# Optimization experiments

Measured on AMD Instinct MI355X. Metric: run time of the kernel, lower is better.

Reference implementation:

```python
import jax, jax.numpy as jnp
import numpy as np
import math

B, L, D, H, DK, DFF = 4, 1024, 1024, 16, 64, 4096
NUM_BUCKETS, MAX_DIST = 32, 128


def _relative_position_bucket(rel):
    # bidirectional T5 bucketing; rel = memory_pos - context_pos
    nb = NUM_BUCKETS // 2
    n = -rel
    ret = (n < 0).astype(jnp.int32) * nb
    n = jnp.abs(n)
    max_exact = nb // 2
    is_small = n < max_exact
    val_if_large = max_exact + (
        jnp.log(jnp.maximum(n, 1).astype(jnp.float32) / max_exact)
        / math.log(MAX_DIST / max_exact)
        * (nb - max_exact)
    ).astype(jnp.int32)
    val_if_large = jnp.minimum(val_if_large, nb - 1)
    return ret + jnp.where(is_small, n.astype(jnp.int32), val_if_large)


def t5_layernorm(x, w, eps):
    # no mean subtraction, no bias (T5 style)
    var = jnp.mean(jnp.square(x.astype(jnp.float32)), axis=-1, keepdims=True)
    return w * (x / jnp.sqrt(var + eps))


def setup_inputs() -> dict:
    key = jax.random.key(0)
    ks = jax.random.split(key, 12)
    inp = {
        "src": jax.random.normal(ks[0], (B, L, D), dtype=jnp.float32),
        "enc_position": jnp.broadcast_to(jnp.arange(L, dtype=jnp.int32), (B, L)),
        "ln1_w": jnp.ones((D,), jnp.float32),
        "wq": jax.random.normal(ks[1], (H * DK, D), jnp.float32) * (D * DK) ** -0.5,
        "bq": jnp.zeros((H * DK,), jnp.float32),
        "wk": jax.random.normal(ks[2], (H * DK, D), jnp.float32) * D ** -0.5,
        "bk": jnp.zeros((H * DK,), jnp.float32),
        "wv": jax.random.normal(ks[3], (H * DK, D), jnp.float32) * D ** -0.5,
        "bv": jnp.zeros((H * DK,), jnp.float32),
        "fc_w": jax.random.normal(ks[4], (D, H * DK), jnp.float32) * (H * DK) ** -0.5,
        "fc_b": jnp.zeros((D,), jnp.float32),
        "rel_bias": jax.random.normal(ks[5], (NUM_BUCKETS, H), jnp.float32) * 0.02,
        "ln2_w": jnp.ones((D,), jnp.float32),
        "wi": jax.random.normal(ks[6], (DFF, D), jnp.float32) * D ** -0.5,
        "wo": jax.random.normal(ks[7], (D, DFF), jnp.float32) * DFF ** -0.5,
    }
    return inp


def reference(src, enc_position, ln1_w, wq, bq, wk, bk, wv, bv, fc_w, fc_b,
              rel_bias, ln2_w, wi, wo):
    b, l, d = src.shape
    temp = DK ** 0.5

    # --- Multi-head self attention (pre-LN, T5 relative bias) ---
    proj = t5_layernorm(src, ln1_w, 1e-12)
    q = (proj @ wq.T + bq).reshape(b, l, H, DK).transpose(0, 2, 1, 3)  # [b,h,l,dk]
    k = (proj @ wk.T + bk).reshape(b, l, H, DK).transpose(0, 2, 1, 3)
    v = (proj @ wv.T + bv).reshape(b, l, H, DK).transpose(0, 2, 1, 3)

    # relative position bias: [b, h, l_q, l_k]
    rel = enc_position[:, None, :] - enc_position[:, :, None]  # mem - ctx
    bucket = _relative_position_bucket(rel)                    # [b, l, l]
    position_bias = rel_bias[bucket].transpose(0, 3, 1, 2)     # [b, h, l, l]

    scores = jnp.einsum("bhqd,bhkd->bhqk", q / temp, k) + position_bias
    attn = jax.nn.softmax(scores, axis=-1)                     # dropout = eval no-op
    ctx = jnp.einsum("bhqk,bhkd->bhqd", attn, v)
    ctx = ctx.transpose(0, 2, 1, 3).reshape(b, l, H * DK)
    attn_out = ctx @ fc_w.T + fc_b + src                       # residual
    attn_sum = jnp.sum(attn, axis=1)                           # [b, l, l]

    # --- Position-wise FFN (pre-LN, gelu, no biases) ---
    nx = t5_layernorm(attn_out, ln2_w, 1e-6)
    h = jax.nn.gelu(nx @ wi.T, approximate=False)
    out = attn_out + h @ wo.T
    return out, attn_sum, position_bias
```

## Files before the change

### kernel.cpp

```cpp
#include <hip/hip_runtime.h>
#include <hip/hip_bf16.h>
#include <math.h>

typedef __attribute__((ext_vector_type(8))) short short8;
typedef __attribute__((ext_vector_type(4))) float f32x4;
typedef unsigned short u16;

#define L2E 1.44269504088896340736f

__device__ __forceinline__ u16 f2bf(float f) {
  union { float f; unsigned u; } x; x.f = f;
  unsigned r = x.u + 0x7fffu + ((x.u >> 16) & 1u);
  return (u16)(r >> 16);
}

__device__ __forceinline__ void gload16(const void* g, void* l) {
  auto gp = reinterpret_cast<const __attribute__((address_space(1))) void*>(
      reinterpret_cast<uintptr_t>(g));
  auto lp = reinterpret_cast<__attribute__((address_space(3))) void*>(
      reinterpret_cast<uintptr_t>(l));
  __builtin_amdgcn_global_load_lds(gp, lp, 16, 0, 0);
}

__device__ __forceinline__ int bucket_fn(int rel) {
  int n = -rel;
  int ret = 0;
  if (n < 0) { ret = 16; n = -n; }
  if (n < 8) return ret + n;
  int e = 31 - __clz(n);
  unsigned nn = (unsigned)n * (unsigned)n;
  int f = 2 * e + ((nn >= (1u << (2 * e + 1))) ? 1 : 0) - 6;
  int val = 8 + f;
  if (val > 15) val = 15;
  return ret + val;
}

__global__ __launch_bounds__(256) void prep(
    const float* __restrict__ wq, const float* __restrict__ wk,
    const float* __restrict__ wv, const float* __restrict__ fcw,
    const float* __restrict__ wi, const float* __restrict__ wo,
    const float* __restrict__ bq, const float* __restrict__ bk,
    const float* __restrict__ bv, const float* __restrict__ rel_bias,
    u16* __restrict__ wqb, u16* __restrict__ wkb, u16* __restrict__ wvb,
    u16* __restrict__ fcwb, u16* __restrict__ wib, u16* __restrict__ wob,
    float* __restrict__ fb, float* __restrict__ tab) {
  const int blk = blockIdx.x, t = threadIdx.x;
  if (blk < 12288) {
    const float* s; u16* d; int rel;
    if (blk < 1024)      { s = wq;  d = wqb;  rel = blk; }
    else if (blk < 2048) { s = wk;  d = wkb;  rel = blk - 1024; }
    else if (blk < 3072) { s = wv;  d = wvb;  rel = blk - 2048; }
    else if (blk < 4096) { s = fcw; d = fcwb; rel = blk - 3072; }
    else if (blk < 8192) { s = wi;  d = wib;  rel = blk - 4096; }
    else                 { s = wo;  d = wob;  rel = blk - 8192; }
    const int i = (rel * 256 + t) * 4;
    float4 v = *(const float4*)&s[i];
    d[i + 0] = f2bf(v.x); d[i + 1] = f2bf(v.y);
    d[i + 2] = f2bf(v.z); d[i + 3] = f2bf(v.w);
  } else if (blk < 12300) {
    const int i = (blk - 12288) * 256 + t;
    fb[i] = i < 1024 ? bq[i] : (i < 2048 ? bk[i - 1024] : bv[i - 2048]);
  } else {
    const int idx = (blk - 12300) * 256 + t;
    const int h = idx >> 11;
    const int rel = (idx & 2047) - 1024;
    tab[idx] = rel_bias[bucket_fn(rel) * 16 + h];
  }
}

__global__ __launch_bounds__(256) void write_pb(const float* __restrict__ tab,
                                                float* __restrict__ pb) {
  const int i = blockIdx.x, h = blockIdx.y, t = threadIdx.x;
  __shared__ float tabs[2048];
  ((float4*)tabs)[t]       = ((const float4*)(tab + h * 2048))[t];
  ((float4*)tabs)[t + 256] = ((const float4*)(tab + h * 2048))[t + 256];
  __syncthreads();
  const int j = t * 4;
  float4 o;
  o.x = tabs[j + 0 - i + 1024];
  o.y = tabs[j + 1 - i + 1024];
  o.z = tabs[j + 2 - i + 1024];
  o.w = tabs[j + 3 - i + 1024];
#pragma unroll
  for (int b = 0; b < 4; b++)
    *(float4*)&pb[(((size_t)(b * 16 + h)) * 1024 + i) * 1024 + j] = o;
}

__global__ __launch_bounds__(256) void t5_ln(const float* __restrict__ x,
                                             const float* __restrict__ wgt,
                                             float eps, u16* __restrict__ out) {
  const int row = blockIdx.x, t = threadIdx.x;
  const float4 v = ((const float4*)(x + (size_t)row * 1024))[t];
  float ss = v.x * v.x + v.y * v.y + v.z * v.z + v.w * v.w;
#pragma unroll
  for (int off = 1; off < 64; off <<= 1) ss += __shfl_xor(ss, off, 64);
  __shared__ float red[4];
  if ((t & 63) == 0) red[t >> 6] = ss;
  __syncthreads();
  float tot = red[0] + red[1] + red[2] + red[3];
  float inv = 1.0f / sqrtf(tot * (1.0f / 1024.0f) + eps);
  const float4 wv = ((const float4*)wgt)[t];
  u16* o = out + (size_t)row * 1024 + t * 4;
  o[0] = f2bf(v.x * inv * wv.x);
  o[1] = f2bf(v.y * inv * wv.y);
  o[2] = f2bf(v.z * inv * wv.z);
  o[3] = f2bf(v.w * inv * wv.w);
}

__global__ __launch_bounds__(256) void transpose_v(const u16* __restrict__ v,
                                                   u16* __restrict__ vt) {
  __shared__ u16 T[64][72];
  const int bh = blockIdx.y;
  const int l0 = blockIdx.x * 64;
  const int t = threadIdx.x;
  const int sr = t >> 3, sc = (t & 7) * 8;
  const u16* vb = v + (size_t)bh * 65536;
  *(short8*)&T[sr][sc]      = *(const short8*)&vb[(size_t)(l0 + sr) * 64 + sc];
  *(short8*)&T[sr + 32][sc] = *(const short8*)&vb[(size_t)(l0 + sr + 32) * 64 + sc];
  __syncthreads();
  u16* vtb = vt + (size_t)bh * 65536;
  short8 o0, o1;
#pragma unroll
  for (int u = 0; u < 8; u++) {
    ((u16*)&o0)[u] = T[sc + u][sr];
    ((u16*)&o1)[u] = T[sc + u][sr + 32];
  }
  *(short8*)&vtb[(size_t)sr * 1024 + l0 + sc]        = o0;
  *(short8*)&vtb[(size_t)(sr + 32) * 1024 + l0 + sc] = o1;
}

template<int MODE>
__global__ __launch_bounds__(256, 2) void gemm_wide(
    const u16* __restrict__ A, const u16* __restrict__ Bw,
    int M, int N, int K,
    const float* __restrict__ bias, float scale, u16* __restrict__ outB) {
  __shared__ u16 As[3][4096];
  __shared__ u16 Bs[3][8192];
  const int t = threadIdx.x;
  const int w = t >> 6, lane = t & 63;
  const int wr = w >> 1, wc = w & 1;
  const int g = lane >> 4, lc = lane & 15;
  const int m0 = blockIdx.y * 128, n0 = blockIdx.x * 256;

  const int srowA = w * 32 + (lane >> 2);
  const int srowB = w * 64 + (lane >> 2);
  const int scA = (lane & 3) ^ ((srowA >> 1) & 3);
  const int scB = (lane & 3) ^ ((srowB >> 1) & 3);
  const u16* Ag = &A[(size_t)(m0 + srowA) * K + scA * 8];
  const u16* Bg = &Bw[(size_t)(n0 + srowB) * K + scB * 8];
  const size_t row16 = (size_t)16 * K;
  const int swz = (lc >> 1) & 3;

  const int NT = K >> 5;
  f32x4 acc[4][8] = {};

  auto stage = [&](int buf, int tt) {
    const int k0 = tt << 5;
    u16* lA = &As[buf][w * 1024];
    u16* lB = &Bs[buf][w * 2048];
    gload16(Ag + k0, lA);
    gload16(Ag + row16 + k0, lA + 512);
    gload16(Bg + k0, lB);
    gload16(Bg + row16 + k0, lB + 512);
    gload16(Bg + 2 * row16 + k0, lB + 1024);
    gload16(Bg + 3 * row16 + k0, lB + 1536);
  };

  stage(0, 0);
  stage(1, 1);

  for (int tt = 0; tt < NT; tt++) {
    const int cur = tt % 3;
    if (tt < NT - 1) {
      asm volatile("s_waitcnt vmcnt(6)" ::: "memory");
    } else {
      asm volatile("s_waitcnt vmcnt(0)" ::: "memory");
    }
    __builtin_amdgcn_s_barrier();
    short8 af[4], bf[8];
#pragma unroll
    for (int mi = 0; mi < 4; mi++)
      af[mi] = *(short8*)&As[cur][(wr * 64 + mi * 16 + lc) * 32 + (g ^ swz) * 8];
#pragma unroll
    for (int ni = 0; ni < 8; ni++)
      bf[ni] = *(short8*)&Bs[cur][(wc * 128 + ni * 16 + lc) * 32 + (g ^ swz) * 8];
    if (tt + 2 < NT) stage((tt + 2) % 3, tt + 2);
    __builtin_amdgcn_s_setprio(1);
#pragma unroll
    for (int mi = 0; mi < 4; mi++)
#pragma unroll
      for (int ni = 0; ni < 8; ni++)
        acc[mi][ni] = __builtin_amdgcn_mfma_f32_16x16x32_bf16(af[mi], bf[ni], acc[mi][ni], 0, 0, 0);
    __builtin_amdgcn_s_setprio(0);
  }

  u16* Es = &As[0][0];
  __syncthreads();
#pragma unroll
  for (int mi = 0; mi < 4; mi++) {
#pragma unroll
    for (int ni = 0; ni < 8; ni++) {
#pragma unroll
      for (int r = 0; r < 4; r++) {
        const int col = n0 + wc * 128 + ni * 16 + lc;
        float v = acc[mi][ni][r];
        if (MODE == 0) {
          v = (v + bias[col]) * ((col >> 10) == 0 ? scale : 1.0f);
        } else {
          v = 0.5f * v * (1.0f + erff(v * 0.70710678118654752440f));
        }
        Es[(wr * 16 + g * 4 + r) * 256 + wc * 128 + ni * 16 + lc] = f2bf(v);
      }
    }
    __syncthreads();
    {
      const int r16 = t >> 4;
      const int cc = (t & 15) * 16;
#pragma unroll
      for (int wr2 = 0; wr2 < 2; wr2++) {
        short8 o0 = *(short8*)&Es[(wr2 * 16 + r16) * 256 + cc];
        short8 o1 = *(short8*)&Es[(wr2 * 16 + r16) * 256 + cc + 8];
        const int row = m0 + wr2 * 64 + mi * 16 + r16;
        if (MODE == 0) {
          const int col0 = n0 + cc;
          const int which = col0 >> 10, c = col0 & 1023;
          const int hh = c >> 6, dk = c & 63;
          const int b = row >> 10, pos = row & 1023;
          u16* dst = outB + (size_t)which * 4194304 +
                     (((size_t)(b * 16 + hh)) * 1024 + pos) * 64 + dk;
          *(short8*)dst = o0;
          *(short8*)(dst + 8) = o1;
        } else {
          u16* dst = outB + (size_t)row * (size_t)N + n0 + cc;
          *(short8*)dst = o0;
          *(short8*)(dst + 8) = o1;
        }
      }
    }
    __syncthreads();
  }
}

template<int MODE>
__global__ __launch_bounds__(256, 3) void gemm_nt(
    const u16* __restrict__ A, const u16* __restrict__ Bw,
    int M, int N, int K,
    const float* __restrict__ bias, const float* __restrict__ res,
    float* __restrict__ outF) {
  __shared__ u16 As[3][4096];
  __shared__ u16 Bs[3][4096];
  const int t = threadIdx.x;
  const int w = t >> 6, lane = t & 63;
  const int wr = w >> 1, wc = w & 1;
  const int g = lane >> 4, lc = lane & 15;
  const int m0 = blockIdx.y * 128, n0 = blockIdx.x * 128;

  const int srow = w * 16 + (lane >> 2);
  const int sc8  = (lane & 3) ^ ((srow >> 1) & 3);
  const u16* Ag = &A[(size_t)(m0 + srow) * K + sc8 * 8];
  const u16* Bg = &Bw[(size_t)(n0 + srow) * K + sc8 * 8];
  const size_t row64 = (size_t)64 * K;
  const int swz = (lc >> 1) & 3;

  const int NT = K >> 5;
  f32x4 acc[4][4] = {};

  auto stage = [&](int buf, int tt) {
    const int k0 = tt << 5;
    u16* lA = &As[buf][w * 512];
    u16* lB = &Bs[buf][w * 512];
    gload16(Ag + k0, lA);
    gload16(Ag + row64 + k0, lA + 2048);
    gload16(Bg + k0, lB);
    gload16(Bg + row64 + k0, lB + 2048);
  };

  stage(0, 0);
  stage(1, 1);

  for (int tt = 0; tt < NT; tt++) {
    const int cur = tt % 3;
    if (tt < NT - 1) {
      asm volatile("s_waitcnt vmcnt(4)" ::: "memory");
    } else {
      asm volatile("s_waitcnt vmcnt(0)" ::: "memory");
    }
    __builtin_amdgcn_s_barrier();
    short8 af[4], bf[4];
#pragma unroll
    for (int mi = 0; mi < 4; mi++)
      af[mi] = *(short8*)&As[cur][(wr * 64 + mi * 16 + lc) * 32 + (g ^ swz) * 8];
#pragma unroll
    for (int ni = 0; ni < 4; ni++)
      bf[ni] = *(short8*)&Bs[cur][(wc * 64 + ni * 16 + lc) * 32 + (g ^ swz) * 8];
    if (tt + 2 < NT) stage((tt + 2) % 3, tt + 2);
    __builtin_amdgcn_s_setprio(1);
#pragma unroll
    for (int mi = 0; mi < 4; mi++)
#pragma unroll
      for (int ni = 0; ni < 4; ni++)
        acc[mi][ni] = __builtin_amdgcn_mfma_f32_16x16x32_bf16(af[mi], bf[ni], acc[mi][ni], 0, 0, 0);
    __builtin_amdgcn_s_setprio(0);
  }

#pragma unroll
  for (int mi = 0; mi < 4; mi++) {
#pragma unroll
    for (int ni = 0; ni < 4; ni++) {
#pragma unroll
      for (int r = 0; r < 4; r++) {
        const int row = m0 + wr * 64 + mi * 16 + g * 4 + r;
        const int col = n0 + wc * 64 + ni * 16 + lc;
        float v = acc[mi][ni][r];
        if (MODE == 1) {
          v += bias[col] + res[(size_t)row * 1024 + col];
        } else {
          v += res[(size_t)row * 1024 + col];
        }
        outF[(size_t)row * 1024 + col] = v;
      }
    }
  }
}

template<int MODE>
__global__ __launch_bounds__(256, 4) void gemm_nt64(
    const u16* __restrict__ A, const u16* __restrict__ Bw,
    int M, int N, int K,
    const float* __restrict__ bias, const float* __restrict__ res,
    float* __restrict__ outF) {
  __shared__ u16 As[3][2048];
  __shared__ u16 Bs[3][4096];
  const int t = threadIdx.x;
  const int w = t >> 6, lane = t & 63;
  const int wr = w >> 1, wc = w & 1;
  const int g = lane >> 4, lc = lane & 15;
  const int m0 = blockIdx.y * 64, n0 = blockIdx.x * 128;

  const int srow = w * 16 + (lane >> 2);
  const int sc8  = (lane & 3) ^ ((srow >> 1) & 3);
  const u16* Ag = &A[(size_t)(m0 + srow) * K + sc8 * 8];
  const u16* Bg = &Bw[(size_t)(n0 + srow) * K + sc8 * 8];
  const size_t row64 = (size_t)64 * K;
  const int swz = (lc >> 1) & 3;

  const int NT = K >> 5;
  f32x4 acc[2][4] = {};

  auto stage = [&](int buf, int tt) {
    const int k0 = tt << 5;
    gload16(Ag + k0, &As[buf][w * 512]);
    gload16(Bg + k0, &Bs[buf][w * 512]);
    gload16(Bg + row64 + k0, &Bs[buf][w * 512 + 2048]);
  };

  stage(0, 0);
  stage(1, 1);

  for (int tt = 0; tt < NT; tt++) {
    const int cur = tt % 3;
    if (tt < NT - 1) {
      asm volatile("s_waitcnt vmcnt(3)" ::: "memory");
    } else {
      asm volatile("s_waitcnt vmcnt(0)" ::: "memory");
    }
    __builtin_amdgcn_s_barrier();
    short8 af[2], bf[4];
#pragma unroll
    for (int mi = 0; mi < 2; mi++)
      af[mi] = *(short8*)&As[cur][(wr * 32 + mi * 16 + lc) * 32 + (g ^ swz) * 8];
#pragma unroll
    for (int ni = 0; ni < 4; ni++)
      bf[ni] = *(short8*)&Bs[cur][(wc * 64 + ni * 16 + lc) * 32 + (g ^ swz) * 8];
    if (tt + 2 < NT) stage((tt + 2) % 3, tt + 2);
    __builtin_amdgcn_s_setprio(1);
#pragma unroll
    for (int mi = 0; mi < 2; mi++)
#pragma unroll
      for (int ni = 0; ni < 4; ni++)
        acc[mi][ni] = __builtin_amdgcn_mfma_f32_16x16x32_bf16(af[mi], bf[ni], acc[mi][ni], 0, 0, 0);
    __builtin_amdgcn_s_setprio(0);
  }

#pragma unroll
  for (int mi = 0; mi < 2; mi++) {
#pragma unroll
    for (int ni = 0; ni < 4; ni++) {
#pragma unroll
      for (int r = 0; r < 4; r++) {
        const int row = m0 + wr * 32 + mi * 16 + g * 4 + r;
        const int col = n0 + wc * 64 + ni * 16 + lc;
        float v = acc[mi][ni][r];
        if (MODE == 1) {
          v += bias[col] + res[(size_t)row * 1024 + col];
        } else {
          v += res[(size_t)row * 1024 + col];
        }
        outF[(size_t)row * 1024 + col] = v;
      }
    }
  }
}

__global__ __launch_bounds__(256) void attn_kernel(
    const u16* __restrict__ q, const u16* __restrict__ k,
    const u16* __restrict__ vt, const float* __restrict__ tab,
    u16* __restrict__ ctx, float* __restrict__ ml) {
  const int bh = blockIdx.y;
  const int h = bh & 15, b = bh >> 4;
  const int i0 = blockIdx.x * 64;
  const int t = threadIdx.x, w = t >> 6, lane = t & 63;
  const int g = lane >> 4, lc = lane & 15;
  const int sr = t >> 3;
  const int swc = ((t & 7) ^ (sr & 7)) * 8;
  const int sc = (t & 7) * 8;

  __shared__ u16 Ks[2][64][64];
  __shared__ u16 Vts[2][64][64];
  __shared__ u16 P[4][16][64];
  __shared__ float tabs[2048];

  const u16* qb  = q + (size_t)bh * 65536;
  const u16* kb  = k + (size_t)bh * 65536;
  const u16* vtb = vt + (size_t)bh * 65536;

  {
    float4 t0 = ((const float4*)(tab + h * 2048))[t];
    float4 t1 = ((const float4*)(tab + h * 2048))[t + 256];
    t0.x *= L2E; t0.y *= L2E; t0.z *= L2E; t0.w *= L2E;
    t1.x *= L2E; t1.y *= L2E; t1.z *= L2E; t1.w *= L2E;
    ((float4*)tabs)[t]       = t0;
    ((float4*)tabs)[t + 256] = t1;
  }

  const short8 aq0 = *(const short8*)&qb[(size_t)(i0 + w * 16 + lc) * 64 + g * 8];
  const short8 aq1 = *(const short8*)&qb[(size_t)(i0 + w * 16 + lc) * 64 + 32 + g * 8];

  {
    short8 ka = *(const short8*)&kb[(size_t)sr * 64 + sc];
    short8 kc = *(const short8*)&kb[(size_t)(sr + 32) * 64 + sc];
    short8 va = *(const short8*)&vtb[(size_t)sr * 1024 + sc];
    short8 vc = *(const short8*)&vtb[(size_t)(sr + 32) * 1024 + sc];
    *(short8*)&Ks[0][sr][swc]       = ka;
    *(short8*)&Ks[0][sr + 32][swc]  = kc;
    *(short8*)&Vts[0][sr][swc]      = va;
    *(short8*)&Vts[0][sr + 32][swc] = vc;
  }
  __syncthreads();

  const int rx = lc & 7;
  const int ibase = 1024 - i0 - (w * 16 + g * 4) + lc;

  float m_r[4] = {-INFINITY, -INFINITY, -INFINITY, -INFINITY};
  float l_r[4] = {0.f, 0.f, 0.f, 0.f};
  f32x4 cacc[4] = {};

  for (int tt = 0; tt < 16; tt++) {
    const int buf = tt & 1;
    const int j0 = tt * 64;

    short8 nka, nkc, nva, nvc;
    if (tt < 15) {
      const int jn = j0 + 64;
      nka = *(const short8*)&kb[(size_t)(jn + sr) * 64 + sc];
      nkc = *(const short8*)&kb[(size_t)(jn + sr + 32) * 64 + sc];
      nva = *(const short8*)&vtb[(size_t)sr * 1024 + jn + sc];
      nvc = *(const short8*)&vtb[(size_t)(sr + 32) * 1024 + jn + sc];
    }

    f32x4 s[4] = {};
#pragma unroll
    for (int ni = 0; ni < 4; ni++) {
      short8 b0 = *(short8*)&Ks[buf][ni * 16 + lc][(g ^ rx) * 8];
      short8 b1 = *(short8*)&Ks[buf][ni * 16 + lc][((4 + g) ^ rx) * 8];
      s[ni] = __builtin_amdgcn_mfma_f32_16x16x32_bf16(aq0, b0, s[ni], 0, 0, 0);
      s[ni] = __builtin_amdgcn_mfma_f32_16x16x32_bf16(aq1, b1, s[ni], 0, 0, 0);
    }
#pragma unroll
    for (int ni = 0; ni < 4; ni++)
#pragma unroll
      for (int r = 0; r < 4; r++)
        s[ni][r] += tabs[ibase + j0 + ni * 16 - r];

#pragma unroll
    for (int r = 0; r < 4; r++) {
      float tm = fmaxf(fmaxf(s[0][r], s[1][r]), fmaxf(s[2][r], s[3][r]));
#pragma unroll
      for (int off = 1; off < 16; off <<= 1) tm = fmaxf(tm, __shfl_xor(tm, off, 64));
      const float mn = fmaxf(m_r[r], tm);
      const float scl = __builtin_amdgcn_exp2f(m_r[r] - mn);
      float rs = 0.f;
#pragma unroll
      for (int ni = 0; ni < 4; ni++) {
        float p = __builtin_amdgcn_exp2f(s[ni][r] - mn);
        s[ni][r] = p;
        rs += p;
      }
#pragma unroll
      for (int off = 1; off < 16; off <<= 1) rs += __shfl_xor(rs, off, 64);
      l_r[r] = l_r[r] * scl + rs;
      m_r[r] = mn;
#pragma unroll
      for (int d = 0; d < 4; d++) cacc[d][r] *= scl;
    }

#pragma unroll
    for (int ni = 0; ni < 4; ni++)
#pragma unroll
      for (int r = 0; r < 4; r++) {
        const int prow = g * 4 + r;
        P[w][prow][(((ni * 2 + (lc >> 3)) ^ (prow & 7)) << 3) | (lc & 7)] = f2bf(s[ni][r]);
      }

    short8 ap0 = *(short8*)&P[w][lc][(g ^ rx) * 8];
    short8 ap1 = *(short8*)&P[w][lc][((4 + g) ^ rx) * 8];
#pragma unroll
    for (int d = 0; d < 4; d++) {
      short8 bv0 = *(short8*)&Vts[buf][d * 16 + lc][(g ^ rx) * 8];
      short8 bv1 = *(short8*)&Vts[buf][d * 16 + lc][((4 + g) ^ rx) * 8];
      cacc[d] = __builtin_amdgcn_mfma_f32_16x16x32_bf16(ap0, bv0, cacc[d], 0, 0, 0);
      cacc[d] = __builtin_amdgcn_mfma_f32_16x16x32_bf16(ap1, bv1, cacc[d], 0, 0, 0);
    }

    if (tt < 15) {
      *(short8*)&Ks[buf ^ 1][sr][swc]       = nka;
      *(short8*)&Ks[buf ^ 1][sr + 32][swc]  = nkc;
      *(short8*)&Vts[buf ^ 1][sr][swc]      = nva;
      *(short8*)&Vts[buf ^ 1][sr + 32][swc] = nvc;
    }
    __syncthreads();
  }

  float inv[4];
#pragma unroll
  for (int r = 0; r < 4; r++) inv[r] = 1.0f / l_r[r];
#pragma unroll
  for (int d = 0; d < 4; d++)
#pragma unroll
    for (int r = 0; r < 4; r++) {
      const int pos = i0 + w * 16 + g * 4 + r;
      ctx[((size_t)b * 1024 + pos) * 1024 + h * 64 + d * 16 + lc] = f2bf(cacc[d][r] * inv[r]);
    }
  if (lc == 0) {
#pragma unroll
    for (int r = 0; r < 4; r++) {
      const int i = i0 + w * 16 + g * 4 + r;
      ml[(size_t)bh * 1024 + i] = m_r[r];
      ml[65536 + (size_t)bh * 1024 + i] = l_r[r];
    }
  }
}

__global__ __launch_bounds__(256) void attn_sum_kernel(
    const u16* __restrict__ q, const u16* __restrict__ k,
    const float* __restrict__ tab, const float* __restrict__ ml,
    float* __restrict__ asum) {
  const int b = blockIdx.z;
  const int i0 = blockIdx.y * 64;
  const int j0 = blockIdx.x * 64;
  const int t = threadIdx.x, w = t >> 6, lane = t & 63;
  const int g = lane >> 4, lc = lane & 15;
  const int sr = t >> 3;
  const int swc = ((t & 7) ^ (sr & 7)) * 8;
  const int sc = (t & 7) * 8;
  const int rx = lc & 7;
  __shared__ u16 Ks[64][64];
  __shared__ float tabs[128];

  f32x4 acc[4] = {};

  for (int h = 0; h < 16; h++) {
    const int bh = b * 16 + h;
    __syncthreads();
    const u16* kb = k + (size_t)bh * 65536;
    *(short8*)&Ks[sr][swc]      = *(const short8*)&kb[(size_t)(j0 + sr) * 64 + sc];
    *(short8*)&Ks[sr + 32][swc] = *(const short8*)&kb[(size_t)(j0 + sr + 32) * 64 + sc];
    if (t < 127) tabs[t] = tab[h * 2048 + (j0 - i0 - 63 + t) + 1024] * L2E;
    __syncthreads();
    const u16* qb = q + (size_t)bh * 65536;
    short8 aq0 = *(const short8*)&qb[(size_t)(i0 + w * 16 + lc) * 64 + g * 8];
    short8 aq1 = *(const short8*)&qb[(size_t)(i0 + w * 16 + lc) * 64 + 32 + g * 8];
    f32x4 s[4] = {};
#pragma unroll
    for (int ni = 0; ni < 4; ni++) {
      short8 b0 = *(short8*)&Ks[ni * 16 + lc][(g ^ rx) * 8];
      short8 b1 = *(short8*)&Ks[ni * 16 + lc][((4 + g) ^ rx) * 8];
      s[ni] = __builtin_amdgcn_mfma_f32_16x16x32_bf16(aq0, b0, s[ni], 0, 0, 0);
      s[ni] = __builtin_amdgcn_mfma_f32_16x16x32_bf16(aq1, b1, s[ni], 0, 0, 0);
    }
    float mm[4], li[4];
#pragma unroll
    for (int r = 0; r < 4; r++) {
      const int i = i0 + w * 16 + g * 4 + r;
      mm[r] = ml[(size_t)bh * 1024 + i];
      li[r] = 1.0f / ml[65536 + (size_t)bh * 1024 + i];
    }
#pragma unroll
    for (int ni = 0; ni < 4; ni++)
#pragma unroll
      for (int r = 0; r < 4; r++) {
        float sv = s[ni][r] + tabs[ni * 16 + lc - w * 16 - g * 4 - r + 63];
        acc[ni][r] += __builtin_amdgcn_exp2f(sv - mm[r]) * li[r];
      }
  }
#pragma unroll
  for (int ni = 0; ni < 4; ni++)
#pragma unroll
    for (int r = 0; r < 4; r++) {
      const int i = i0 + w * 16 + g * 4 + r;
      asum[((size_t)b * 1024 + i) * 1024 + j0 + ni * 16 + lc] = acc[ni][r];
    }
}

extern "C" void kernel_launch(void* const* d_in, const int* in_sizes, int n_in,
                              void* d_out, int out_size, void* d_ws, size_t ws_size,
                              hipStream_t stream) {
  const float* src      = (const float*)d_in[0];
  const float* ln1_w    = (const float*)d_in[2];
  const float* wq       = (const float*)d_in[3];
  const float* bq       = (const float*)d_in[4];
  const float* wk       = (const float*)d_in[5];
  const float* bk       = (const float*)d_in[6];
  const float* wv       = (const float*)d_in[7];
  const float* bv       = (const float*)d_in[8];
  const float* fc_w     = (const float*)d_in[9];
  const float* fc_b     = (const float*)d_in[10];
  const float* rel_bias = (const float*)d_in[11];
  const float* ln2_w    = (const float*)d_in[12];
  const float* wi       = (const float*)d_in[13];
  const float* wo       = (const float*)d_in[14];

  const size_t MB = 1u << 20;
  char* ws = (char*)d_ws;
  u16* wq_b   = (u16*)(ws + 0 * MB);
  u16* wk_b   = (u16*)(ws + 2 * MB);
  u16* wv_b   = (u16*)(ws + 4 * MB);
  u16* fcw_b  = (u16*)(ws + 6 * MB);
  u16* wi_b   = (u16*)(ws + 8 * MB);
  u16* wo_b   = (u16*)(ws + 16 * MB);
  u16* proj_b = (u16*)(ws + 24 * MB);
  u16* q_b    = (u16*)(ws + 32 * MB);
  u16* k_b    = (u16*)(ws + 40 * MB);
  u16* v_b    = (u16*)(ws + 48 * MB);
  u16* vt_b   = (u16*)(ws + 56 * MB);
  u16* h_b    = (u16*)(ws + 32 * MB);
  u16* ctx_b  = (u16*)(ws + 64 * MB);
  float* attn_out = (float*)(ws + 72 * MB);
  float* ml   = (float*)(ws + 88 * MB);
  float* tab  = (float*)(ws + 88 * MB + 512 * 1024);
  float* fb   = (float*)(ws + 90 * MB);

  float* outF = (float*)d_out;
  float* asum = outF + 4194304;
  float* pb   = outF + 8388608;

  prep<<<12428, 256, 0, stream>>>(wq, wk, wv, fc_w, wi, wo, bq, bk, bv, rel_bias,
                                  wq_b, wk_b, wv_b, fcw_b, wi_b, wo_b, fb, tab);

  write_pb<<<dim3(1024, 16), 256, 0, stream>>>(tab, pb);

  t5_ln<<<4096, 256, 0, stream>>>(src, ln1_w, 1e-12f, proj_b);

  gemm_wide<0><<<dim3(12, 32), 256, 0, stream>>>(proj_b, wq_b, 4096, 3072, 1024,
                                                 fb, 0.125f * L2E, q_b);

  transpose_v<<<dim3(16, 64), 256, 0, stream>>>(v_b, vt_b);
  attn_kernel<<<dim3(16, 64), 256, 0, stream>>>(q_b, k_b, vt_b, tab, ctx_b, ml);
  attn_sum_kernel<<<dim3(16, 16, 4), 256, 0, stream>>>(q_b, k_b, tab, ml, asum);

  gemm_nt64<1><<<dim3(8, 64), 256, 0, stream>>>(ctx_b, fcw_b, 4096, 1024, 1024, fc_b, src, attn_out);

  t5_ln<<<4096, 256, 0, stream>>>(attn_out, ln2_w, 1e-6f, proj_b);

  gemm_wide<2><<<dim3(16, 32), 256, 0, stream>>>(proj_b, wi_b, 4096, 4096, 1024,
                                                 nullptr, 1.0f, h_b);
  gemm_nt<3><<<dim3(8, 32), 256, 0, stream>>>(h_b, wo_b, 4096, 1024, 4096,
                                              nullptr, attn_out, outF);
}
```

Before: 382.9 us.

## Retile QKV and FFN-down GEMMs, drop setprio in MFMA loops

The QKV projection moves from the 128x256 wide GEMM to a 128x128 tile kernel with a bf16 head-scatter epilogue staged through LDS, which doubles the block count from 384 to 768 for better CU occupancy. The FFN down-projection switches from 128x128 tiles to 64x128 tiles (512 blocks instead of 256) to improve load balance on a K=4096 GEMM. The s_setprio hints around the MFMA loops are removed. Smaller tiles cost more global traffic for operand reloads.

```diff
diff --git a/kernel.cpp b/kernel.cpp
--- a/kernel.cpp
+++ b/kernel.cpp
@@ -130,6 +130,111 @@
 }
 
 template<int MODE>
+__global__ __launch_bounds__(256, 3) void gemm_nt(
+    const u16* __restrict__ A, const u16* __restrict__ Bw,
+    int M, int N, int K,
+    const float* __restrict__ bias, const float* __restrict__ res,
+    float scale, float* __restrict__ outF, u16* __restrict__ outB) {
+  __shared__ u16 As[3][4096];
+  __shared__ u16 Bs[3][4096];
+  const int t = threadIdx.x;
+  const int w = t >> 6, lane = t & 63;
+  const int wr = w >> 1, wc = w & 1;
+  const int g = lane >> 4, lc = lane & 15;
+  const int m0 = blockIdx.y * 128, n0 = blockIdx.x * 128;
+
+  const int srow = w * 16 + (lane >> 2);
+  const int sc8  = (lane & 3) ^ ((srow >> 1) & 3);
+  const u16* Ag = &A[(size_t)(m0 + srow) * K + sc8 * 8];
+  const u16* Bg = &Bw[(size_t)(n0 + srow) * K + sc8 * 8];
+  const size_t row64 = (size_t)64 * K;
+  const int swz = (lc >> 1) & 3;
+
+  const int NT = K >> 5;
+  f32x4 acc[4][4] = {};
+
+  auto stage = [&](int buf, int tt) {
+    const int k0 = tt << 5;
+    u16* lA = &As[buf][w * 512];
+    u16* lB = &Bs[buf][w * 512];
+    gload16(Ag + k0, lA);
+    gload16(Ag + row64 + k0, lA + 2048);
+    gload16(Bg + k0, lB);
+    gload16(Bg + row64 + k0, lB + 2048);
+  };
+
+  stage(0, 0);
+  stage(1, 1);
+
+  for (int tt = 0; tt < NT; tt++) {
+    const int cur = tt % 3;
+    if (tt < NT - 1) {
+      asm volatile("s_waitcnt vmcnt(4)" ::: "memory");
+    } else {
+      asm volatile("s_waitcnt vmcnt(0)" ::: "memory");
+    }
+    __builtin_amdgcn_s_barrier();
+    short8 af[4], bf[4];
+#pragma unroll
+    for (int mi = 0; mi < 4; mi++)
+      af[mi] = *(short8*)&As[cur][(wr * 64 + mi * 16 + lc) * 32 + (g ^ swz) * 8];
+#pragma unroll
+    for (int ni = 0; ni < 4; ni++)
+      bf[ni] = *(short8*)&Bs[cur][(wc * 64 + ni * 16 + lc) * 32 + (g ^ swz) * 8];
+    if (tt + 2 < NT) stage((tt + 2) % 3, tt + 2);
+#pragma unroll
+    for (int mi = 0; mi < 4; mi++)
+#pragma unroll
+      for (int ni = 0; ni < 4; ni++)
+        acc[mi][ni] = __builtin_amdgcn_mfma_f32_16x16x32_bf16(af[mi], bf[ni], acc[mi][ni], 0, 0, 0);
+  }
+
+  u16* Es = &As[0][0];
+  __syncthreads();
+#pragma unroll
+  for (int mi = 0; mi < 4; mi++) {
+#pragma unroll
+    for (int ni = 0; ni < 4; ni++) {
+#pragma unroll
+      for (int r = 0; r < 4; r++) {
+        const int col = n0 + wc * 64 + ni * 16 + lc;
+        float v = acc[mi][ni][r];
+        if (MODE == 0) {
+          v = (v + bias[col]) * ((col >> 10) == 0 ? scale : 1.0f);
+        } else {
+          v = 0.5f * v * (1.0f + erff(v * 0.70710678118654752440f));
+        }
+        Es[wr * 2048 + (g * 4 + r) * 128 + wc * 64 + ni * 16 + lc] = f2bf(v);
+      }
+    }
+    __syncthreads();
+    {
+      const int rr = t >> 3;
+      const int wr2 = rr >> 4, r16 = rr & 15;
+      const int cc = (t & 7) * 16;
+      short8 o0 = *(short8*)&Es[wr2 * 2048 + r16 * 128 + cc];
+      short8 o1 = *(short8*)&Es[wr2 * 2048 + r16 * 128 + cc + 8];
+      const int row = m0 + wr2 * 64 + mi * 16 + r16;
+      if (MODE == 0) {
+        const int col0 = n0 + cc;
+        const int which = col0 >> 10, c = col0 & 1023;
+        const int hh = c >> 6, dk = c & 63;
+        const int b = row >> 10, pos = row & 1023;
+        u16* dst = outB + (size_t)which * 4194304 +
+                   (((size_t)(b * 16 + hh)) * 1024 + pos) * 64 + dk;
+        *(short8*)dst = o0;
+        *(short8*)(dst + 8) = o1;
+      } else {
+        u16* dst = outB + (size_t)row * (size_t)N + n0 + cc;
+        *(short8*)dst = o0;
+        *(short8*)(dst + 8) = o1;
+      }
+    }
+    __syncthreads();
+  }
+}
+
+template<int MODE>
 __global__ __launch_bounds__(256, 2) void gemm_wide(
     const u16* __restrict__ A, const u16* __restrict__ Bw,
     int M, int N, int K,
@@ -221,105 +326,12 @@
         short8 o0 = *(short8*)&Es[(wr2 * 16 + r16) * 256 + cc];
         short8 o1 = *(short8*)&Es[(wr2 * 16 + r16) * 256 + cc + 8];
         const int row = m0 + wr2 * 64 + mi * 16 + r16;
-        if (MODE == 0) {
-          const int col0 = n0 + cc;
-          const int which = col0 >> 10, c = col0 & 1023;
-          const int hh = c >> 6, dk = c & 63;
-          const int b = row >> 10, pos = row & 1023;
-          u16* dst = outB + (size_t)which * 4194304 +
-                     (((size_t)(b * 16 + hh)) * 1024 + pos) * 64 + dk;
-          *(short8*)dst = o0;
-          *(short8*)(dst + 8) = o1;
-        } else {
-          u16* dst = outB + (size_t)row * (size_t)N + n0 + cc;
-          *(short8*)dst = o0;
-          *(short8*)(dst + 8) = o1;
-        }
+        u16* dst = outB + (size_t)row * (size_t)N + n0 + cc;
+        *(short8*)dst = o0;
+        *(short8*)(dst + 8) = o1;
       }
     }
     __syncthreads();
-  }
-}
-
-template<int MODE>
-__global__ __launch_bounds__(256, 3) void gemm_nt(
-    const u16* __restrict__ A, const u16* __restrict__ Bw,
-    int M, int N, int K,
-    const float* __restrict__ bias, const float* __restrict__ res,
-    float* __restrict__ outF) {
-  __shared__ u16 As[3][4096];
-  __shared__ u16 Bs[3][4096];
-  const int t = threadIdx.x;
-  const int w = t >> 6, lane = t & 63;
-  const int wr = w >> 1, wc = w & 1;
-  const int g = lane >> 4, lc = lane & 15;
-  const int m0 = blockIdx.y * 128, n0 = blockIdx.x * 128;
-
-  const int srow = w * 16 + (lane >> 2);
-  const int sc8  = (lane & 3) ^ ((srow >> 1) & 3);
-  const u16* Ag = &A[(size_t)(m0 + srow) * K + sc8 * 8];
-  const u16* Bg = &Bw[(size_t)(n0 + srow) * K + sc8 * 8];
-  const size_t row64 = (size_t)64 * K;
-  const int swz = (lc >> 1) & 3;
-
-  const int NT = K >> 5;
-  f32x4 acc[4][4] = {};
-
-  auto stage = [&](int buf, int tt) {
-    const int k0 = tt << 5;
-    u16* lA = &As[buf][w * 512];
-    u16* lB = &Bs[buf][w * 512];
-    gload16(Ag + k0, lA);
-    gload16(Ag + row64 + k0, lA + 2048);
-    gload16(Bg + k0, lB);
-    gload16(Bg + row64 + k0, lB + 2048);
-  };
-
-  stage(0, 0);
-  stage(1, 1);
-
-  for (int tt = 0; tt < NT; tt++) {
-    const int cur = tt % 3;
-    if (tt < NT - 1) {
-      asm volatile("s_waitcnt vmcnt(4)" ::: "memory");
-    } else {
-      asm volatile("s_waitcnt vmcnt(0)" ::: "memory");
-    }
-    __builtin_amdgcn_s_barrier();
-    short8 af[4], bf[4];
-#pragma unroll
-    for (int mi = 0; mi < 4; mi++)
-      af[mi] = *(short8*)&As[cur][(wr * 64 + mi * 16 + lc) * 32 + (g ^ swz) * 8];
-#pragma unroll
-    for (int ni = 0; ni < 4; ni++)
-      bf[ni] = *(short8*)&Bs[cur][(wc * 64 + ni * 16 + lc) * 32 + (g ^ swz) * 8];
-    if (tt + 2 < NT) stage((tt + 2) % 3, tt + 2);
-    __builtin_amdgcn_s_setprio(1);
-#pragma unroll
-    for (int mi = 0; mi < 4; mi++)
-#pragma unroll
-      for (int ni = 0; ni < 4; ni++)
-        acc[mi][ni] = __builtin_amdgcn_mfma_f32_16x16x32_bf16(af[mi], bf[ni], acc[mi][ni], 0, 0, 0);
-    __builtin_amdgcn_s_setprio(0);
-  }
-
-#pragma unroll
-  for (int mi = 0; mi < 4; mi++) {
-#pragma unroll
-    for (int ni = 0; ni < 4; ni++) {
-#pragma unroll
-      for (int r = 0; r < 4; r++) {
-        const int row = m0 + wr * 64 + mi * 16 + g * 4 + r;
-        const int col = n0 + wc * 64 + ni * 16 + lc;
-        float v = acc[mi][ni][r];
-        if (MODE == 1) {
-          v += bias[col] + res[(size_t)row * 1024 + col];
-        } else {
-          v += res[(size_t)row * 1024 + col];
-        }
-        outF[(size_t)row * 1024 + col] = v;
-      }
-    }
   }
 }
 
@@ -373,13 +385,11 @@
     for (int ni = 0; ni < 4; ni++)
       bf[ni] = *(short8*)&Bs[cur][(wc * 64 + ni * 16 + lc) * 32 + (g ^ swz) * 8];
     if (tt + 2 < NT) stage((tt + 2) % 3, tt + 2);
-    __builtin_amdgcn_s_setprio(1);
 #pragma unroll
     for (int mi = 0; mi < 2; mi++)
 #pragma unroll
       for (int ni = 0; ni < 4; ni++)
         acc[mi][ni] = __builtin_amdgcn_mfma_f32_16x16x32_bf16(af[mi], bf[ni], acc[mi][ni], 0, 0, 0);
-    __builtin_amdgcn_s_setprio(0);
   }
 
 #pragma unroll
@@ -661,8 +671,8 @@
 
   t5_ln<<<4096, 256, 0, stream>>>(src, ln1_w, 1e-12f, proj_b);
 
-  gemm_wide<0><<<dim3(12, 32), 256, 0, stream>>>(proj_b, wq_b, 4096, 3072, 1024,
-                                                 fb, 0.125f * L2E, q_b);
+  gemm_nt<0><<<dim3(24, 32), 256, 0, stream>>>(proj_b, wq_b, 4096, 3072, 1024, fb, nullptr,
+                                               0.125f * L2E, nullptr, q_b);
 
   transpose_v<<<dim3(16, 64), 256, 0, stream>>>(v_b, vt_b);
   attn_kernel<<<dim3(16, 64), 256, 0, stream>>>(q_b, k_b, vt_b, tab, ctx_b, ml);
@@ -674,6 +684,5 @@
 
   gemm_wide<2><<<dim3(16, 32), 256, 0, stream>>>(proj_b, wi_b, 4096, 4096, 1024,
                                                  nullptr, 1.0f, h_b);
-  gemm_nt<3><<<dim3(8, 32), 256, 0, stream>>>(h_b, wo_b, 4096, 1024, 4096,
-                                              nullptr, attn_out, outF);
-}
+  gemm_nt64<3><<<dim3(8, 64), 256, 0, stream>>>(h_b, wo_b, 4096, 1024, 4096, nullptr, attn_out, outF);
+}
```

After: 371.3 us. 3.1% less time.
